# Kernel tuning notes

Measured on AMD Instinct MI355X. Metric: run time of the kernel, lower is better.

The kernel has to match this reference:

```python
import jax, jax.numpy as jnp
import numpy as np

N, G, E, H, Z = 50000, 2000, 800000, 512, 64
BN_EPS = 1e-5


def setup_inputs() -> dict:
    key = jax.random.key(0)
    ks = jax.random.split(key, 10)
    x = jax.random.normal(ks[0], (N, G), dtype=jnp.float32)
    edge_index = jax.random.randint(ks[1], (2, E), 0, N, dtype=jnp.int32)
    s1 = 1.0 / np.sqrt(G)
    s2 = 1.0 / np.sqrt(H)
    return {
        "x": x,
        "edge_index": edge_index,
        "W1l": jax.random.normal(ks[2], (G, H), dtype=jnp.float32) * s1,
        "b1": jnp.zeros((H,), jnp.float32),
        "W1r": jax.random.normal(ks[3], (G, H), dtype=jnp.float32) * s1,
        "bn_gamma": jax.random.uniform(ks[4], (H,), dtype=jnp.float32) + 0.5,
        "bn_beta": jax.random.normal(ks[5], (H,), dtype=jnp.float32) * 0.1,
        "bn_mean": jax.random.normal(ks[6], (H,), dtype=jnp.float32) * 0.1,
        "bn_var": jax.random.uniform(ks[7], (H,), dtype=jnp.float32) + 0.5,
        "W2l": jax.random.normal(ks[8], (H, Z), dtype=jnp.float32) * s2,
        "b2": jnp.zeros((Z,), jnp.float32),
        "W2r": jax.random.normal(ks[9], (H, Z), dtype=jnp.float32) * s2,
    }


def _sage_conv(h, src, dst, Wl, bl, Wr, n_nodes):
    # mean aggregation of source features at destination nodes
    msg = h[src]  # [E, D] gather
    agg = jax.ops.segment_sum(msg, dst, num_segments=n_nodes)
    cnt = jax.ops.segment_sum(jnp.ones((src.shape[0],), h.dtype), dst, num_segments=n_nodes)
    agg = agg / jnp.maximum(cnt, 1.0)[:, None]
    # PyG SAGEConv: lin_l(agg) + lin_r(x), bias only on lin_l
    return agg @ Wl + bl + h @ Wr


def reference(x, edge_index, W1l, b1, W1r, bn_gamma, bn_beta, bn_mean, bn_var, W2l, b2, W2r):
    src, dst = edge_index[0], edge_index[1]
    n = x.shape[0]
    h = _sage_conv(x, src, dst, W1l, b1, W1r, n)  # [N, H]
    # BatchNorm1d (eval mode: running stats) + ReLU; dropout is identity at inference
    h = (h - bn_mean) * (bn_gamma / jnp.sqrt(bn_var + BN_EPS)) + bn_beta
    h = jax.nn.relu(h)
    z = _sage_conv(h, src, dst, W2l, b2, W2r, n)  # [N, Z]
    return z
```

## Files before the change

kernel.cpp:

```cpp
#include <hip/hip_runtime.h>
#include <hip/hip_bf16.h>


#define BN_EPS 1e-5f
#define GK 2000
#define KP 2048
#define NT1 63
#define NT2 16

typedef __attribute__((ext_vector_type(8))) short bf16x8;
typedef __attribute__((ext_vector_type(4))) float f32x4;
typedef unsigned short u16x8 __attribute__((ext_vector_type(8)));

__device__ inline unsigned short f2bf(float f) {
    union { float f; unsigned u; } v; v.f = f;
    unsigned r = (v.u + 0x7fffu + ((v.u >> 16) & 1u)) >> 16;
    return (unsigned short)r;
}
__device__ inline unsigned short f2bf_hw(float f) {
    __hip_bfloat16 h = __float2bfloat16(f);
    return *reinterpret_cast<unsigned short*>(&h);
}
__device__ inline float bf2f(unsigned short u) {
    union { unsigned u; float f; } v; v.u = ((unsigned)u) << 16;
    return v.f;
}

#define GLL16(gp, lp) __builtin_amdgcn_global_load_lds( \
    (const __attribute__((address_space(1))) void*)(gp), \
    (__attribute__((address_space(3))) void*)(lp), 16, 0, 0)

__global__ __launch_bounds__(256) void prep_fused(
    const float* __restrict__ W1l, const float* __restrict__ W1r,
    const float* __restrict__ gamma, const float* __restrict__ beta,
    const float* __restrict__ mean, const float* __restrict__ var,
    const float* __restrict__ b1, unsigned short* __restrict__ BT,
    const float* __restrict__ W2l, const float* __restrict__ W2r,
    unsigned short* __restrict__ BT2, float* __restrict__ b1p,
    const int* __restrict__ ei, int* __restrict__ cnt, int E)
{
    const int bb = blockIdx.x;
    if (bb < 1024) {
        int idx = bb * 256 + threadIdx.x;
        int c  = idx >> 8;
        int k0 = (idx & 255) << 3;
        int cc = (c < 512) ? c : c - 512;
        float scv = gamma[cc] * rsqrtf(var[cc] + BN_EPS);
        const float* W = (c < 512) ? (W1l + cc) : (W1r + cc);
        unsigned short us[8];
#pragma unroll
        for (int j = 0; j < 8; ++j) {
            int k = k0 + j;
            float v = (k < GK) ? W[(size_t)k * 512] * scv : 0.0f;
            us[j] = f2bf(v);
        }
        *(u16x8*)&BT[(size_t)c * KP + k0] = *(u16x8*)us;
    } else if (bb < 1056) {
        int idx = (bb - 1024) * 256 + threadIdx.x;
        int c  = idx >> 6;
        int k0 = (idx & 63) << 3;
        const float* W = (c < 64) ? (W2l + c) : (W2r + (c - 64));
        unsigned short us[8];
#pragma unroll
        for (int j = 0; j < 8; ++j) us[j] = f2bf(W[(size_t)(k0 + j) * 64]);
        *(u16x8*)&BT2[(size_t)c * 512 + k0] = *(u16x8*)us;
    } else if (bb == 1056) {
#pragma unroll
        for (int h = 0; h < 2; ++h) {
            int c = threadIdx.x + h * 256;
            float scv = gamma[c] * rsqrtf(var[c] + BN_EPS);
            b1p[c] = b1[c] * scv + (beta[c] - mean[c] * scv);
        }
    } else {
        for (int i = (bb - 1057) * 256 + threadIdx.x; i < E; i += 1024 * 256)
            atomicAdd(&cnt[ei[E + i]], 1);
    }
}

__global__ __launch_bounds__(1024) void scan_kernel(const int* __restrict__ cnt,
                                                    int* __restrict__ row_start, int n) {
    __shared__ int part[1024];
    int t = threadIdx.x;
    int chunk = (n + 1023) >> 10;
    int lo = t * chunk;
    int hi = lo + chunk; if (hi > n) hi = n;
    int s = 0;
    for (int i = lo; i < hi; ++i) s += cnt[i];
    part[t] = s;
    __syncthreads();
    for (int off = 1; off < 1024; off <<= 1) {
        int add = (t >= off) ? part[t - off] : 0;
        __syncthreads();
        part[t] += add;
        __syncthreads();
    }
    int run = (t == 0) ? 0 : part[t - 1];
    for (int i = lo; i < hi; ++i) { row_start[i] = run; run += cnt[i]; }
    if (t == 1023) row_start[n] = part[1023];
}

__global__ void fill_kernel(const int* __restrict__ ei, int E,
                            const int* __restrict__ row_start,
                            int* __restrict__ cnt, int* __restrict__ colidx) {
    int i = blockIdx.x * blockDim.x + threadIdx.x;
    if (i < E) {
        int d = ei[E + i];
        int p = atomicSub(&cnt[d], 1) - 1;
        colidx[row_start[d] + p] = ei[i];
    }
}

__global__ __launch_bounds__(512) void gemm1_256(
    const float* __restrict__ x, int M,
    const unsigned short* __restrict__ BT,
    unsigned short* __restrict__ Y)
{
    __shared__ __align__(16) float          As[3][8192];
    __shared__ __align__(16) unsigned short Bs[3][8192];

    const int t = threadIdx.x, wid = t >> 6, lane = t & 63;
    const int nbr = (M + 255) >> 8;
    const int nwg = nbr * 4;
    const int b   = blockIdx.x;
    int swz;
    if ((nwg & 7) == 0) swz = (b & 7) * (nwg >> 3) + (b >> 3);
    else swz = b;
    const int row0 = (swz >> 2) << 8;
    const int col0 = (swz & 3) << 8;

    int   cA[4];
    const float* aP[4];
    int   aOmax[4];
#pragma unroll
    for (int j = 0; j < 4; ++j) {
        int c = t + 512 * j;
        cA[j] = c;
        int row = row0 + (c >> 3); if (row >= M) row = M - 1;
        int g = (c & 7) ^ ((c >> 3) & 7);
        aP[j] = x + (size_t)row * GK + g * 4;
        aOmax[j] = 1996 - g * 4;
    }

    const int cb0 = t, cb1 = t + 512;
    const int gb0 = ((cb0 & 3) ^ ((cb0 >> 3) & 3)) << 3;
    const int gb1 = ((cb1 & 3) ^ ((cb1 >> 3) & 3)) << 3;
    const unsigned short* bS0 = BT + (size_t)(col0 + (cb0 >> 2)) * KP + gb0;
    const unsigned short* bS1 = BT + (size_t)(col0 + (cb1 >> 2)) * KP + gb1;

    const int wr = wid >> 2, wc = wid & 3;
    const int fr16 = lane & 15;
    const int gswr = ((lane >> 4) ^ ((fr16 >> 1) & 3)) << 4;
    const int offA0 = (((lane >> 4) * 2) ^ (fr16 & 7)) << 4;
    const int offA1 = offA0 ^ 16;

    f32x4 acc[8][4];
#pragma unroll
    for (int m = 0; m < 8; ++m)
#pragma unroll
        for (int n = 0; n < 4; ++n) acc[m][n] = (f32x4)0.0f;

#define STG(kt, buf) do {                                               \
        float* ab_ = &As[buf][0];                                       \
        unsigned short* bb_ = &Bs[buf][0];                              \
        _Pragma("unroll")                                               \
        for (int j_ = 0; j_ < 4; ++j_) {                                \
            int o_ = (kt) * 32; if (o_ > aOmax[j_]) o_ = aOmax[j_];     \
            GLL16(aP[j_] + o_, ab_ + cA[j_] * 4);                       \
        }                                                               \
        GLL16(bS0 + (size_t)(kt) * 32, bb_ + cb0 * 8);                  \
        GLL16(bS1 + (size_t)(kt) * 32, bb_ + cb1 * 8);                  \
    } while (0)

    STG(0, 0);
    STG(1, 1);

    int rb = 0;
    for (int it = 0; it < NT1; ++it) {
        if (it == NT1 - 1) {
            asm volatile("s_waitcnt vmcnt(0)" ::: "memory");
        } else {
            asm volatile("s_waitcnt vmcnt(6)" ::: "memory");
        }
        __builtin_amdgcn_s_barrier();
        __builtin_amdgcn_sched_barrier(0);

        const char* Ab = (const char*)&As[rb][0];
        const char* Bb = (const char*)&Bs[rb][0];

        bf16x8 af[8], bfr[4];
#pragma unroll
        for (int m = 0; m < 8; ++m) {
            int rowb = (wr * 128 + m * 16 + fr16) << 7;
            f32x4 lo = *(const f32x4*)(Ab + rowb + offA0);
            f32x4 hi = *(const f32x4*)(Ab + rowb + offA1);
            unsigned short us[8];
            us[0] = f2bf_hw(lo[0]); us[1] = f2bf_hw(lo[1]);
            us[2] = f2bf_hw(lo[2]); us[3] = f2bf_hw(lo[3]);
            us[4] = f2bf_hw(hi[0]); us[5] = f2bf_hw(hi[1]);
            us[6] = f2bf_hw(hi[2]); us[7] = f2bf_hw(hi[3]);
            af[m] = *(bf16x8*)us;
        }
#pragma unroll
        for (int n = 0; n < 4; ++n)
            bfr[n] = *(const bf16x8*)(Bb + ((wc * 64 + n * 16 + fr16) << 6) + gswr);

        if (it + 2 < NT1) {
            int wb = rb + 2; if (wb >= 3) wb -= 3;
            STG(it + 2, wb);
        }

        __builtin_amdgcn_s_setprio(1);
#pragma unroll
        for (int m = 0; m < 8; ++m)
#pragma unroll
            for (int n = 0; n < 4; ++n)
                acc[m][n] = __builtin_amdgcn_mfma_f32_16x16x32_bf16(
                    af[m], bfr[n], acc[m][n], 0, 0, 0);
        __builtin_amdgcn_s_setprio(0);

        rb = (rb == 2) ? 0 : rb + 1;
    }
#undef STG

    const int crow = (lane >> 4) << 2;
#pragma unroll
    for (int m = 0; m < 8; ++m) {
        int rbase = row0 + wr * 128 + m * 16 + crow;
#pragma unroll
        for (int r = 0; r < 4; ++r) {
            int row = rbase + r;
            if (row < M) {
                unsigned short* Yp = Y + (size_t)row * 1024 + col0 + wc * 64 + fr16;
#pragma unroll
                for (int n = 0; n < 4; ++n)
                    Yp[n * 16] = f2bf(acc[m][n][r]);
            }
        }
    }
}

__global__ __launch_bounds__(256) void agg1_kernel(
    const unsigned short* __restrict__ Y, unsigned short* __restrict__ Hh,
    const int* __restrict__ row_start, const int* __restrict__ colidx,
    const float* __restrict__ b1p, int n)
{
    int wid  = (blockIdx.x * blockDim.x + threadIdx.x) >> 6;
    int lane = threadIdx.x & 63;
    if (wid >= n) return;
    int c0 = lane * 8;
    float bb[8];
    *(float4*)&bb[0] = *(const float4*)&b1p[c0];
    *(float4*)&bb[4] = *(const float4*)&b1p[c0 + 4];

    int s0 = row_start[wid], s1 = row_start[wid + 1];
    float acc[8] = {0, 0, 0, 0, 0, 0, 0, 0};
    int i = s0;
    for (; i + 2 <= s1; i += 2) {
        int src0 = colidx[i], src1 = colidx[i + 1];
        u16x8 v0 = *(const u16x8*)&Y[(size_t)src0 * 1024 + c0];
        u16x8 v1 = *(const u16x8*)&Y[(size_t)src1 * 1024 + c0];
#pragma unroll
        for (int j = 0; j < 8; ++j) acc[j] += bf2f(v0[j]) + bf2f(v1[j]);
    }
    if (i < s1) {
        int src = colidx[i];
        u16x8 v = *(const u16x8*)&Y[(size_t)src * 1024 + c0];
#pragma unroll
        for (int j = 0; j < 8; ++j) acc[j] += bf2f(v[j]);
    }
    float inv = 1.0f / fmaxf((float)(s1 - s0), 1.0f);
    u16x8 sv = *(const u16x8*)&Y[(size_t)wid * 1024 + 512 + c0];
    unsigned short o[8];
#pragma unroll
    for (int j = 0; j < 8; ++j) {
        float pre = acc[j] * inv + bb[j] + bf2f(sv[j]);
        o[j] = f2bf(fmaxf(pre, 0.0f));
    }
    *(u16x8*)&Hh[(size_t)wid * 512 + c0] = *(u16x8*)o;
}

__global__ __launch_bounds__(256) void gemm2_bf16(
    const unsigned short* __restrict__ Hh, int M,
    const unsigned short* __restrict__ BT2,
    unsigned short* __restrict__ U)
{
    __shared__ __align__(16) unsigned short As[2][128][32];
    __shared__ __align__(16) unsigned short Bs[2][128][32];

    const int t    = threadIdx.x;
    const int wid  = t >> 6;
    const int lane = t & 63;
    const int row0 = blockIdx.x << 7;

    const int c_lo = wid * 64 + lane;
    const int c_hi = c_lo + 256;
    const int s_lo = ((c_lo & 3) ^ ((c_lo >> 3) & 3)) << 3;
    const int s_hi = ((c_hi & 3) ^ ((c_hi >> 3) & 3)) << 3;
    int ra = row0 + (c_lo >> 2); if (ra >= M) ra = M - 1;
    int rbw = row0 + (c_hi >> 2); if (rbw >= M) rbw = M - 1;
    const unsigned short* aSrc0 = Hh + (size_t)ra * 512 + s_lo;
    const unsigned short* aSrc1 = Hh + (size_t)rbw * 512 + s_hi;
    const unsigned short* bSrc0 = BT2 + (size_t)(c_lo >> 2) * 512 + s_lo;
    const unsigned short* bSrc1 = BT2 + (size_t)(c_hi >> 2) * 512 + s_hi;

    const int wr   = wid >> 1, wc = wid & 1;
    const int fr16 = lane & 15;
    const int gsw2 = ((lane >> 4) ^ ((fr16 >> 1) & 3)) << 4;

    f32x4 acc[4][4];
#pragma unroll
    for (int m = 0; m < 4; ++m)
#pragma unroll
        for (int n = 0; n < 4; ++n) acc[m][n] = (f32x4)0.0f;

#define STAGE2(kt, buf) do {                                                  \
        int ko = (kt) * 32;                                                   \
        GLL16(aSrc0 + ko, (unsigned short*)&As[buf][0][0] + (size_t)c_lo * 8);  \
        GLL16(aSrc1 + ko, (unsigned short*)&As[buf][0][0] + (size_t)c_hi * 8);  \
        GLL16(bSrc0 + ko, (unsigned short*)&Bs[buf][0][0] + (size_t)c_lo * 8);  \
        GLL16(bSrc1 + ko, (unsigned short*)&Bs[buf][0][0] + (size_t)c_hi * 8);  \
    } while (0)

    STAGE2(0, 0);
    int cur = 0;
    for (int it = 0; it < NT2; ++it) {
        __syncthreads();
        if (it + 1 < NT2) STAGE2(it + 1, cur ^ 1);

        const char* Ab = (const char*)&As[cur][0][0];
        const char* Bb = (const char*)&Bs[cur][0][0];
        bf16x8 af[4], bfr[4];
#pragma unroll
        for (int m = 0; m < 4; ++m)
            af[m] = *(const bf16x8*)(Ab + ((wr * 64 + m * 16 + fr16) << 6) + gsw2);
#pragma unroll
        for (int n = 0; n < 4; ++n)
            bfr[n] = *(const bf16x8*)(Bb + ((wc * 64 + n * 16 + fr16) << 6) + gsw2);
#pragma unroll
        for (int m = 0; m < 4; ++m)
#pragma unroll
            for (int n = 0; n < 4; ++n)
                acc[m][n] = __builtin_amdgcn_mfma_f32_16x16x32_bf16(
                    af[m], bfr[n], acc[m][n], 0, 0, 0);
        cur ^= 1;
    }
#undef STAGE2

    const int crow = (lane >> 4) << 2;
#pragma unroll
    for (int m = 0; m < 4; ++m) {
        int rbase = row0 + wr * 64 + m * 16 + crow;
#pragma unroll
        for (int r = 0; r < 4; ++r) {
            int row = rbase + r;
            if (row < M) {
                unsigned short* Up = U + (size_t)row * 128 + wc * 64 + fr16;
#pragma unroll
                for (int n = 0; n < 4; ++n)
                    Up[n * 16] = f2bf(acc[m][n][r]);
            }
        }
    }
}

__global__ __launch_bounds__(256) void agg2_kernel(
    const unsigned short* __restrict__ U,
    const int* __restrict__ row_start, const int* __restrict__ colidx,
    const float* __restrict__ b2, float* __restrict__ out, int n)
{
    int wid  = (blockIdx.x * blockDim.x + threadIdx.x) >> 6;
    int lane = threadIdx.x & 63;
    if (wid >= n) return;
    int s0 = row_start[wid], s1 = row_start[wid + 1];
    float acc = 0.f;
    int i = s0;
    for (; i + 2 <= s1; i += 2) {
        int src0 = colidx[i], src1 = colidx[i + 1];
        acc += bf2f(U[(size_t)src0 * 128 + lane]) + bf2f(U[(size_t)src1 * 128 + lane]);
    }
    if (i < s1) acc += bf2f(U[(size_t)colidx[i] * 128 + lane]);
    float inv = 1.0f / fmaxf((float)(s1 - s0), 1.0f);
    float z = acc * inv + b2[lane] + bf2f(U[(size_t)wid * 128 + 64 + lane]);
    out[(size_t)wid * 64 + lane] = z;
}

extern "C" void kernel_launch(void* const* d_in, const int* in_sizes, int n_in,
                              void* d_out, int out_size, void* d_ws, size_t ws_size,
                              hipStream_t stream) {
    const float* x     = (const float*)d_in[0];
    const int*   ei    = (const int*)d_in[1];
    const float* W1l   = (const float*)d_in[2];
    const float* b1    = (const float*)d_in[3];
    const float* W1r   = (const float*)d_in[4];
    const float* gamma = (const float*)d_in[5];
    const float* beta  = (const float*)d_in[6];
    const float* mean  = (const float*)d_in[7];
    const float* var   = (const float*)d_in[8];
    const float* W2l   = (const float*)d_in[9];
    const float* b2    = (const float*)d_in[10];
    const float* W2r   = (const float*)d_in[11];
    float* out = (float*)d_out;

    const int N = in_sizes[0] / 2000;
    const int E = in_sizes[1] / 2;
    const int nby = (N + 127) / 128;

    char* ws = (char*)d_ws;
    unsigned short* Y   = (unsigned short*)ws;
    unsigned short* Hh  = Y + (size_t)N * 1024;
    unsigned short* BT  = Hh + (size_t)N * 512;
    unsigned short* BT2 = BT + (size_t)1024 * KP;
    float* b1p     = (float*)(BT2 + (size_t)128 * 512);
    int* cnt       = (int*)(b1p + 512);
    int* row_start = cnt + N;
    int* colidx    = row_start + N + 4;
    unsigned short* U = Y;

    hipMemsetAsync(cnt, 0, (size_t)N * sizeof(int), stream);

    prep_fused<<<2081, 256, 0, stream>>>(
        W1l, W1r, gamma, beta, mean, var, b1, BT, W2l, W2r, BT2, b1p,
        ei, cnt, E);

    scan_kernel<<<1, 1024, 0, stream>>>(cnt, row_start, N);
    int eb = (E + 255) / 256;
    fill_kernel<<<eb, 256, 0, stream>>>(ei, E, row_start, cnt, colidx);

    int nbr = (N + 255) / 256;
    gemm1_256<<<nbr * 4, 512, 0, stream>>>(x, N, BT, Y);
    agg1_kernel<<<(N + 3) / 4, 256, 0, stream>>>(
        Y, Hh, row_start, colidx, b1p, N);
    gemm2_bf16<<<nby, 256, 0, stream>>>(Hh, N, BT2, U);
    agg2_kernel<<<(N + 3) / 4, 256, 0, stream>>>(
        U, row_start, colidx, b2, out, N);
}
```

Measured before the change: 691.4 us.

## Pre-convert x to padded bf16 in a fused conversion/CSR-fill kernel before GEMM1

Adds a pass that converts the fp32 input x into a zero-padded bf16 buffer (K padded to 2048), fused into the same launch as the CSR fill kernel. GEMM1 then loads bf16 A tiles straight into LDS, halving A-tile LDS footprint and removing the per-iteration fp32-to-bf16 conversion from the inner loop. The cost is an extra full read of x plus a write and reread of the 200MB bf16 copy. The workspace is rearranged so Hh reuses the xb region.

```diff
diff --git a/kernel.cpp b/kernel.cpp
--- a/kernel.cpp
+++ b/kernel.cpp
@@ -1,11 +1,10 @@
 #include <hip/hip_runtime.h>
-#include <hip/hip_bf16.h>
 
 
 #define BN_EPS 1e-5f
 #define GK 2000
 #define KP 2048
-#define NT1 63
+#define NT1 64
 #define NT2 16
 
 typedef __attribute__((ext_vector_type(8))) short bf16x8;
@@ -16,10 +15,6 @@
     union { float f; unsigned u; } v; v.f = f;
     unsigned r = (v.u + 0x7fffu + ((v.u >> 16) & 1u)) >> 16;
     return (unsigned short)r;
-}
-__device__ inline unsigned short f2bf_hw(float f) {
-    __hip_bfloat16 h = __float2bfloat16(f);
-    return *reinterpret_cast<unsigned short*>(&h);
 }
 __device__ inline float bf2f(unsigned short u) {
     union { unsigned u; float f; } v; v.u = ((unsigned)u) << 16;
@@ -99,23 +94,45 @@
     if (t == 1023) row_start[n] = part[1023];
 }
 
-__global__ void fill_kernel(const int* __restrict__ ei, int E,
-                            const int* __restrict__ row_start,
-                            int* __restrict__ cnt, int* __restrict__ colidx) {
-    int i = blockIdx.x * blockDim.x + threadIdx.x;
-    if (i < E) {
-        int d = ei[E + i];
-        int p = atomicSub(&cnt[d], 1) - 1;
-        colidx[row_start[d] + p] = ei[i];
+__global__ __launch_bounds__(256) void convfill_kernel(
+    const float* __restrict__ x, unsigned short* __restrict__ xb, int N,
+    const int* __restrict__ ei, int E, const int* __restrict__ row_start,
+    int* __restrict__ cnt, int* __restrict__ colidx)
+{
+    const int bb = blockIdx.x;
+    if (bb < 2048) {
+        const int total8 = N * 256;
+        for (int idx = bb * 256 + threadIdx.x; idx < total8; idx += 2048 * 256) {
+            int row = idx >> 8;
+            int k8  = idx & 255;
+            unsigned short us[8];
+            if (k8 < 250) {
+                const float4* p = (const float4*)(x + (size_t)row * 2000 + k8 * 8);
+                float4 v0 = p[0], v1 = p[1];
+                us[0]=f2bf(v0.x); us[1]=f2bf(v0.y); us[2]=f2bf(v0.z); us[3]=f2bf(v0.w);
+                us[4]=f2bf(v1.x); us[5]=f2bf(v1.y); us[6]=f2bf(v1.z); us[7]=f2bf(v1.w);
+            } else {
+#pragma unroll
+                for (int j = 0; j < 8; ++j) us[j] = 0;
+            }
+            *(u16x8*)&xb[(size_t)row * 2048 + k8 * 8] = *(u16x8*)us;
+        }
+    } else {
+        int i = (bb - 2048) * 256 + threadIdx.x;
+        if (i < E) {
+            int d = ei[E + i];
+            int p = atomicSub(&cnt[d], 1) - 1;
+            colidx[row_start[d] + p] = ei[i];
+        }
     }
 }
 
 __global__ __launch_bounds__(512) void gemm1_256(
-    const float* __restrict__ x, int M,
+    const unsigned short* __restrict__ xb, int M,
     const unsigned short* __restrict__ BT,
     unsigned short* __restrict__ Y)
 {
-    __shared__ __align__(16) float          As[3][8192];
+    __shared__ __align__(16) unsigned short As[3][8192];
     __shared__ __align__(16) unsigned short Bs[3][8192];
 
     const int t = threadIdx.x, wid = t >> 6, lane = t & 63;
@@ -128,30 +145,19 @@
     const int row0 = (swz >> 2) << 8;
     const int col0 = (swz & 3) << 8;
 
-    int   cA[4];
-    const float* aP[4];
-    int   aOmax[4];
-#pragma unroll
-    for (int j = 0; j < 4; ++j) {
-        int c = t + 512 * j;
-        cA[j] = c;
-        int row = row0 + (c >> 3); if (row >= M) row = M - 1;
-        int g = (c & 7) ^ ((c >> 3) & 7);
-        aP[j] = x + (size_t)row * GK + g * 4;
-        aOmax[j] = 1996 - g * 4;
-    }
-
-    const int cb0 = t, cb1 = t + 512;
-    const int gb0 = ((cb0 & 3) ^ ((cb0 >> 3) & 3)) << 3;
-    const int gb1 = ((cb1 & 3) ^ ((cb1 >> 3) & 3)) << 3;
-    const unsigned short* bS0 = BT + (size_t)(col0 + (cb0 >> 2)) * KP + gb0;
-    const unsigned short* bS1 = BT + (size_t)(col0 + (cb1 >> 2)) * KP + gb1;
+    const int c0 = t, c1 = t + 512;
+    const int g0 = ((c0 & 3) ^ ((c0 >> 3) & 3)) << 3;
+    const int g1 = ((c1 & 3) ^ ((c1 >> 3) & 3)) << 3;
+    int ra0 = row0 + (c0 >> 2); if (ra0 >= M) ra0 = M - 1;
+    int ra1 = row0 + (c1 >> 2); if (ra1 >= M) ra1 = M - 1;
+    const unsigned short* aS0 = xb + (size_t)ra0 * KP + g0;
+    const unsigned short* aS1 = xb + (size_t)ra1 * KP + g1;
+    const unsigned short* bS0 = BT + (size_t)(col0 + (c0 >> 2)) * KP + g0;
+    const unsigned short* bS1 = BT + (size_t)(col0 + (c1 >> 2)) * KP + g1;
 
     const int wr = wid >> 2, wc = wid & 3;
     const int fr16 = lane & 15;
     const int gswr = ((lane >> 4) ^ ((fr16 >> 1) & 3)) << 4;
-    const int offA0 = (((lane >> 4) * 2) ^ (fr16 & 7)) << 4;
-    const int offA1 = offA0 ^ 16;
 
     f32x4 acc[8][4];
 #pragma unroll
@@ -159,16 +165,13 @@
 #pragma unroll
         for (int n = 0; n < 4; ++n) acc[m][n] = (f32x4)0.0f;
 
-#define STG(kt, buf) do {                                               \
-        float* ab_ = &As[buf][0];                                       \
-        unsigned short* bb_ = &Bs[buf][0];                              \
-        _Pragma("unroll")                                               \
-        for (int j_ = 0; j_ < 4; ++j_) {                                \
-            int o_ = (kt) * 32; if (o_ > aOmax[j_]) o_ = aOmax[j_];     \
-            GLL16(aP[j_] + o_, ab_ + cA[j_] * 4);                       \
-        }                                                               \
-        GLL16(bS0 + (size_t)(kt) * 32, bb_ + cb0 * 8);                  \
-        GLL16(bS1 + (size_t)(kt) * 32, bb_ + cb1 * 8);                  \
+#define STG(kt, buf) do {                                          \
+        unsigned short* ab_ = &As[buf][0];                         \
+        unsigned short* bb_ = &Bs[buf][0];                         \
+        GLL16(aS0 + (size_t)(kt) * 32, ab_ + c0 * 8);              \
+        GLL16(aS1 + (size_t)(kt) * 32, ab_ + c1 * 8);              \
+        GLL16(bS0 + (size_t)(kt) * 32, bb_ + c0 * 8);              \
+        GLL16(bS1 + (size_t)(kt) * 32, bb_ + c1 * 8);              \
     } while (0)
 
     STG(0, 0);
@@ -179,27 +182,17 @@
         if (it == NT1 - 1) {
             asm volatile("s_waitcnt vmcnt(0)" ::: "memory");
         } else {
-            asm volatile("s_waitcnt vmcnt(6)" ::: "memory");
+            asm volatile("s_waitcnt vmcnt(4)" ::: "memory");
         }
         __builtin_amdgcn_s_barrier();
         __builtin_amdgcn_sched_barrier(0);
 
         const char* Ab = (const char*)&As[rb][0];
         const char* Bb = (const char*)&Bs[rb][0];
-
         bf16x8 af[8], bfr[4];
 #pragma unroll
-        for (int m = 0; m < 8; ++m) {
-            int rowb = (wr * 128 + m * 16 + fr16) << 7;
-            f32x4 lo = *(const f32x4*)(Ab + rowb + offA0);
-            f32x4 hi = *(const f32x4*)(Ab + rowb + offA1);
-            unsigned short us[8];
-            us[0] = f2bf_hw(lo[0]); us[1] = f2bf_hw(lo[1]);
-            us[2] = f2bf_hw(lo[2]); us[3] = f2bf_hw(lo[3]);
-            us[4] = f2bf_hw(hi[0]); us[5] = f2bf_hw(hi[1]);
-            us[6] = f2bf_hw(hi[2]); us[7] = f2bf_hw(hi[3]);
-            af[m] = *(bf16x8*)us;
-        }
+        for (int m = 0; m < 8; ++m)
+            af[m] = *(const bf16x8*)(Ab + ((wr * 128 + m * 16 + fr16) << 6) + gswr);
 #pragma unroll
         for (int n = 0; n < 4; ++n)
             bfr[n] = *(const bf16x8*)(Bb + ((wc * 64 + n * 16 + fr16) << 6) + gswr);
@@ -406,15 +399,16 @@
     const int nby = (N + 127) / 128;
 
     char* ws = (char*)d_ws;
-    unsigned short* Y   = (unsigned short*)ws;
-    unsigned short* Hh  = Y + (size_t)N * 1024;
-    unsigned short* BT  = Hh + (size_t)N * 512;
+    unsigned short* xb  = (unsigned short*)ws;
+    unsigned short* Y   = xb + (size_t)N * KP;
+    unsigned short* BT  = Y + (size_t)N * 1024;
     unsigned short* BT2 = BT + (size_t)1024 * KP;
     float* b1p     = (float*)(BT2 + (size_t)128 * 512);
     int* cnt       = (int*)(b1p + 512);
     int* row_start = cnt + N;
     int* colidx    = row_start + N + 4;
-    unsigned short* U = Y;
+    unsigned short* Hh = xb;
+    unsigned short* U  = Y;
 
     hipMemsetAsync(cnt, 0, (size_t)N * sizeof(int), stream);
 
@@ -423,11 +417,13 @@
         ei, cnt, E);
 
     scan_kernel<<<1, 1024, 0, stream>>>(cnt, row_start, N);
+
     int eb = (E + 255) / 256;
-    fill_kernel<<<eb, 256, 0, stream>>>(ei, E, row_start, cnt, colidx);
+    convfill_kernel<<<2048 + eb, 256, 0, stream>>>(
+        x, xb, N, ei, E, row_start, cnt, colidx);
 
     int nbr = (N + 255) / 256;
-    gemm1_256<<<nbr * 4, 512, 0, stream>>>(x, N, BT, Y);
+    gemm1_256<<<nbr * 4, 512, 0, stream>>>(xb, N, BT, Y);
     agg1_kernel<<<(N + 3) / 4, 256, 0, stream>>>(
         Y, Hh, row_start, colidx, b1p, N);
     gemm2_bf16<<<nby, 256, 0, stream>>>(Hh, N, BT2, U);
```

Result: no change. 694.1 us (+0.4%).
